# Kernel optimization log

Hardware: AMD Instinct MI355X
Metric: run time of the kernel (lower is better)

The kernel has to match this reference:

```python
import jax, jax.numpy as jnp
import numpy as np

N = 10000        # num_nodes
F_IN = 256       # dataset_num_features
H = 128          # hidden_channels
C_OUT = 40       # dataset_num_classes
L = 3            # num_layers
HEADS = 8
DH = H // HEADS  # per-head dim
E = 160000       # num edges (before self loops)
SCALE = 1.0 / float(np.sqrt(DH))


def setup_inputs() -> dict:
    key = jax.random.key(0)
    ks = jax.random.split(key, 8)
    s = lambda k, *sh: (jax.random.normal(k, sh, dtype=jnp.float32) * 0.05)
    return dict(
        edge_index=jax.random.randint(ks[0], (2, E), 0, N, dtype=jnp.int32),
        x_param=s(ks[1], N, F_IN),
        lin1_w=s(ks[2], F_IN, H),
        lin1_b=jnp.zeros((H,), jnp.float32),
        wq=s(ks[3], L, H, H),
        wk=s(ks[4], L, H, H),
        wv=s(ks[5], L, H, H),
        bq=jnp.zeros((L, H), jnp.float32),
        bk=jnp.zeros((L, H), jnp.float32),
        bv=jnp.zeros((L, H), jnp.float32),
        lin2_w=s(ks[6], H, C_OUT),
        lin2_b=jnp.zeros((C_OUT,), jnp.float32),
    )


def _gcn_norm(edge_index):
    # PyG gcn_norm: add self loops (weight 1), symmetric D^-1/2 A D^-1/2
    loops = jnp.arange(N, dtype=edge_index.dtype)
    row = jnp.concatenate([edge_index[0], loops])  # source j
    col = jnp.concatenate([edge_index[1], loops])  # target i
    deg = jax.ops.segment_sum(jnp.ones(row.shape, jnp.float32), col, num_segments=N)
    dis = jnp.where(deg > 0, jax.lax.rsqrt(jnp.maximum(deg, 1e-12)), 0.0)
    return row, col, dis[row] * dis[col]


def _restricted_softmax(score):
    # softmax with an implicit extra logit at `margin=0`
    m = jnp.maximum(jnp.max(score, axis=-1, keepdims=True), 0.0)
    e = jnp.exp(score - m)
    return e / (jnp.sum(e, axis=-1, keepdims=True) + jnp.exp(-m))


def _forward(edge_index, x_param, lin1_w, lin1_b, wq, wk, wv, bq, bk, bv, lin2_w, lin2_b):
    row, col, norm = _gcn_norm(edge_index)
    # dropouts are eval-mode no-ops
    x = jax.nn.relu(x_param @ lin1_w + lin1_b)  # [N, H]
    x_all = x[:, None, :]                       # [N, 1, H]
    for l in range(L):
        t = x_all.shape[1]
        # project per-node first (linear commutes with per-edge gather)
        q = (x_all[:, -1] @ wq[l] + bq[l]).reshape(N, HEADS, DH)      # query from latest state
        k = (x_all @ wk[l] + bk[l]).reshape(N, t, HEADS, DH)          # keys over full history
        v = (x_all @ wv[l] + bv[l]).reshape(N, t, HEADS, DH)
        qe = q[col]   # [Etot, heads, dh]   (x_i)
        ke = k[row]   # [Etot, t, heads, dh] (x_j)
        ve = v[row]
        score = jnp.einsum('ehd,ethd->eht', qe, ke) * SCALE
        attn = _restricted_softmax(score)        # attention-dropout is a no-op in eval
        msg = jnp.einsum('eht,ethd->ehd', attn, ve).reshape(-1, H) * norm[:, None]
        out = jax.ops.segment_sum(msg, col, num_segments=N)  # aggr='add'
        x = jax.nn.relu(out)
        x_all = jnp.concatenate([x_all, x[:, None, :]], axis=1)
    logits = x_all[:, -1] @ lin2_w + lin2_b
    return jax.nn.log_softmax(logits, axis=1)


def reference(edge_index, x_param, lin1_w, lin1_b, wq, wk, wv, bq, bk, bv, lin2_w, lin2_b):
    return _forward(edge_index, x_param, lin1_w, lin1_b, wq, wk, wv, bq, bk, bv, lin2_w, lin2_b)
```

## Files before the change

### kernel.cpp

```cpp
#include <hip/hip_runtime.h>
#include <math.h>

#define N_NODES 10000
#define F_IN_D  256
#define H_DIM   128
#define C_OUTD  40
#define NHEADS  8
#define NEDGES  160000
#define ETOT    (NEDGES + N_NODES)
#define SCALE_F 0.25f
#define TILES_N 157
#define KVSZ    ((size_t)N_NODES * 3 * 256)

typedef __attribute__((ext_vector_type(8))) short bf16x8;
typedef __attribute__((ext_vector_type(4))) float f32x4;
typedef __attribute__((ext_vector_type(2))) float f32x2;

__device__ __forceinline__ unsigned short f2bf(float f) {
    unsigned int u = __float_as_uint(f);
    unsigned int r = (u + 0x7FFFu + ((u >> 16) & 1u)) >> 16;
    return (unsigned short)r;
}
__device__ __forceinline__ unsigned char f2fp8(float v) {
    int pk = __builtin_amdgcn_cvt_pk_fp8_f32(v, v, 0, false);
    return (unsigned char)(pk & 0xff);
}


__global__ void k_prep(const float* __restrict__ w1, const float* __restrict__ wq,
                       const float* __restrict__ wk, const float* __restrict__ wv,
                       const float* __restrict__ w2, const int* __restrict__ col,
                       unsigned short* __restrict__ W1T, unsigned short* __restrict__ WTq,
                       unsigned short* __restrict__ WTk, unsigned short* __restrict__ WTv,
                       unsigned short* __restrict__ W2T, int* __restrict__ degi,
                       int* __restrict__ cursor) {
    int b = blockIdx.x;
    if (b < 768) {
        int e = b * 256 + threadIdx.x;
        if (e < 32768) {
            int n = e >> 8, k = e & 255;
            W1T[e] = f2bf(w1[k * H_DIM + n]);
        } else if (e < 180224) {
            int e2 = e - 32768;
            int mat = e2 >> 14;
            int r   = e2 & 16383;
            int n = r >> 7, k = r & 127;
            int l = mat / 3, ws = mat % 3;
            const float*    src = (ws == 0) ? wq  : (ws == 1) ? wk  : wv;
            unsigned short* dst = (ws == 0) ? WTq : (ws == 1) ? WTk : WTv;
            dst[l * 16384 + n * H_DIM + k] = f2bf(src[l * 16384 + k * H_DIM + n]);
        } else if (e < 186368) {
            int e3 = e - 180224;
            int c = e3 >> 7, k = e3 & 127;
            W2T[c * H_DIM + k] = (c < C_OUTD) ? f2bf(w2[k * C_OUTD + c]) : 0;
        } else if (e < 196368) {
            cursor[e - 186368] = 0;
        }
    } else {
        int e = (b - 768) * 256 + threadIdx.x;
        if (e < NEDGES) atomicAdd(&degi[col[e]], 1);
    }
}


__device__ __forceinline__ void lin1_block(int bid, int ct0, const float* __restrict__ X,
                                           const unsigned short* __restrict__ W1T,
                                           const float* __restrict__ b1,
                                           unsigned short* __restrict__ X0, int nct) {
    int tid = threadIdx.x;
    int wid = tid >> 6, lane = tid & 63;
    int m = lane & 15, quad = lane >> 4;
    int rowA = bid * 64 + wid * 16 + m;
    int rowc = rowA < N_NODES ? rowA : N_NODES - 1;
    bf16x8 af[8];
    const float* ap = X + (size_t)rowc * F_IN_D + quad * 8;
    #pragma unroll
    for (int s = 0; s < 8; ++s) {
        float4 lo = *(const float4*)(ap + s * 32);
        float4 hi = *(const float4*)(ap + s * 32 + 4);
        union { unsigned short u[8]; bf16x8 v; } pk;
        pk.u[0] = f2bf(lo.x); pk.u[1] = f2bf(lo.y);
        pk.u[2] = f2bf(lo.z); pk.u[3] = f2bf(lo.w);
        pk.u[4] = f2bf(hi.x); pk.u[5] = f2bf(hi.y);
        pk.u[6] = f2bf(hi.z); pk.u[7] = f2bf(hi.w);
        af[s] = pk.v;
    }
    int row0 = bid * 64 + wid * 16 + quad * 4;
    for (int ct = ct0; ct < ct0 + nct; ++ct) {
        int col = ct * 16 + m;
        const unsigned short* bp = W1T + (size_t)col * F_IN_D + quad * 8;
        f32x4 acc = {0.f, 0.f, 0.f, 0.f};
        #pragma unroll
        for (int s = 0; s < 8; ++s) {
            bf16x8 bfr = __builtin_bit_cast(bf16x8, *(const uint4*)(bp + s * 32));
            acc = __builtin_amdgcn_mfma_f32_16x16x32_bf16(af[s], bfr, acc, 0, 0, 0);
        }
        float bb = b1[col];
        #pragma unroll
        for (int rg = 0; rg < 4; ++rg) {
            int r = row0 + rg;
            if (r < N_NODES)
                X0[(size_t)r * H_DIM + col] = f2bf(fmaxf(acc[rg] + bb, 0.f));
        }
    }
}

__device__ __forceinline__ void qkv_block(int mi, int rt,
                                          const unsigned short* __restrict__ XHb,
                                          const unsigned short* __restrict__ WTq_l,
                                          const unsigned short* __restrict__ WTk_l,
                                          const unsigned short* __restrict__ WTv_l,
                                          const float* __restrict__ bq_l,
                                          const float* __restrict__ bk_l,
                                          const float* __restrict__ bv_l,
                                          unsigned short* __restrict__ Qb,
                                          unsigned char* __restrict__ KVb,
                                          int hasQ, int qslice, int nK, int sbase, int nct) {
    int tid = threadIdx.x;
    int wid = tid >> 6, lane = tid & 63;
    int m = lane & 15, quad = lane >> 4;
    const unsigned short* WT; const float* bias; int slice, mode;
    if (hasQ && mi == 0) { WT = WTq_l; bias = bq_l; slice = qslice; mode = 0; }
    else {
        int j = mi - hasQ;
        if (j < nK) { WT = WTk_l; bias = bk_l; slice = sbase + j;      mode = 1; }
        else        { WT = WTv_l; bias = bv_l; slice = sbase + j - nK; mode = 2; }
    }
    const unsigned short* A = XHb + (size_t)slice * N_NODES * H_DIM;
    int rowA = rt * 64 + wid * 16 + m;
    bf16x8 af[4];
    const unsigned short* ap = A + (size_t)rowA * H_DIM + quad * 8;
    #pragma unroll
    for (int s = 0; s < 4; ++s)
        af[s] = __builtin_bit_cast(bf16x8, *(const uint4*)(ap + s * 32));
    int row0 = rt * 64 + wid * 16 + quad * 4;
    int vofs = (mode == 2) ? 8 : 0;
    for (int cp = 0; cp < nct; ++cp) {
        int colA = cp * 32 + m;
        int colB = colA + 16;
        const unsigned short* bpA = WT + (size_t)colA * H_DIM + quad * 8;
        const unsigned short* bpB = WT + (size_t)colB * H_DIM + quad * 8;
        bf16x8 bA[4], bB[4];
        #pragma unroll
        for (int s = 0; s < 4; ++s) {
            bA[s] = __builtin_bit_cast(bf16x8, *(const uint4*)(bpA + s * 32));
            bB[s] = __builtin_bit_cast(bf16x8, *(const uint4*)(bpB + s * 32));
        }
        f32x4 accA = {0.f, 0.f, 0.f, 0.f};
        f32x4 accB = {0.f, 0.f, 0.f, 0.f};
        #pragma unroll
        for (int s = 0; s < 4; ++s) {
            accA = __builtin_amdgcn_mfma_f32_16x16x32_bf16(af[s], bA[s], accA, 0, 0, 0);
            accB = __builtin_amdgcn_mfma_f32_16x16x32_bf16(af[s], bB[s], accB, 0, 0, 0);
        }
        float bbA = bias[colA], bbB = bias[colB];
        #pragma unroll
        for (int rg = 0; rg < 4; ++rg) {
            int r = row0 + rg;
            if (r < N_NODES) {
                float vA = accA[rg] + bbA;
                float vB = accB[rg] + bbB;
                if (mode == 0) {
                    Qb[(size_t)r * H_DIM + colA] = f2bf(vA * SCALE_F);
                    Qb[(size_t)r * H_DIM + colB] = f2bf(vB * SCALE_F);
                } else {
                    size_t nb = ((size_t)r * 3 + slice) * 256;
                    KVb[nb + (colA >> 3) * 16 + (colA & 7) + vofs] = f2fp8(vA);
                    KVb[nb + (colB >> 3) * 16 + (colB & 7) + vofs] = f2fp8(vB);
                }
            }
        }
    }
}


template <int T>
__device__ __forceinline__ void kv_load(const uint4* __restrict__ KV, int r, int ci,
                                        uint4 (&kv)[T]) {
    const uint4* p = KV + (size_t)r * 48 + ci;
    #pragma unroll
    for (int s = 0; s < T; ++s) kv[s] = p[s * 16];
}

template <int T>
__device__ __forceinline__ void edge_accum(const uint4 (&kv)[T], const float (&q)[8],
                                           float nrm, float (&a)[8]) {
    float den = 1.f;
    float mv[8];
    #pragma unroll
    for (int i = 0; i < 8; ++i) mv[i] = 0.f;
    #pragma unroll
    for (int s = 0; s < T; ++s) {
        f32x2 k0 = __builtin_amdgcn_cvt_pk_f32_fp8(kv[s].x, false);
        f32x2 k1 = __builtin_amdgcn_cvt_pk_f32_fp8(kv[s].x, true);
        f32x2 k2 = __builtin_amdgcn_cvt_pk_f32_fp8(kv[s].y, false);
        f32x2 k3 = __builtin_amdgcn_cvt_pk_f32_fp8(kv[s].y, true);
        float p = q[0] * k0[0] + q[1] * k0[1] + q[2] * k1[0] + q[3] * k1[1]
                + q[4] * k2[0] + q[5] * k2[1] + q[6] * k3[0] + q[7] * k3[1];
        p += __shfl_xor(p, 1, 2);
        float w = __expf(p);
        den += w;
        f32x2 v0 = __builtin_amdgcn_cvt_pk_f32_fp8(kv[s].z, false);
        f32x2 v1 = __builtin_amdgcn_cvt_pk_f32_fp8(kv[s].z, true);
        f32x2 v2 = __builtin_amdgcn_cvt_pk_f32_fp8(kv[s].w, false);
        f32x2 v3 = __builtin_amdgcn_cvt_pk_f32_fp8(kv[s].w, true);
        mv[0] += w * v0[0]; mv[1] += w * v0[1];
        mv[2] += w * v1[0]; mv[3] += w * v1[1];
        mv[4] += w * v2[0]; mv[5] += w * v2[1];
        mv[6] += w * v3[0]; mv[7] += w * v3[1];
    }
    float ws = __fdividef(nrm, den);
    #pragma unroll
    for (int i = 0; i < 8; ++i) a[i] += ws * mv[i];
}

template <int T>
__device__ __forceinline__ void attn_block(int bid, const unsigned short* __restrict__ Q,
                                           const uint4* __restrict__ KV,
                                           const int2* __restrict__ csr,
                                           const int* __restrict__ degi,
                                           unsigned int* __restrict__ Xout) {
    int tid = threadIdx.x;
    int wid = tid >> 6, lane = tid & 63;
    int quarter = lane >> 4, ci = lane & 15;
    int n = bid * 4 + wid;

    int cnt = degi[n] + 1;
    if (cnt > 64) cnt = 64;
    int li = lane < cnt ? lane : cnt - 1;
    int2 eAll = csr[(n << 6) + li];
    int   rAll = eAll.x;
    float nAll = (lane < cnt) ? __int_as_float(eAll.y) : 0.f;

    float q[8];
    {
        uint4 qp = *(const uint4*)&Q[(size_t)n * H_DIM + ci * 8];
        q[0] = __uint_as_float(qp.x << 16);
        q[1] = __uint_as_float(qp.x & 0xffff0000u);
        q[2] = __uint_as_float(qp.y << 16);
        q[3] = __uint_as_float(qp.y & 0xffff0000u);
        q[4] = __uint_as_float(qp.z << 16);
        q[5] = __uint_as_float(qp.z & 0xffff0000u);
        q[6] = __uint_as_float(qp.w << 16);
        q[7] = __uint_as_float(qp.w & 0xffff0000u);
    }
    int nq = (cnt + 3) >> 2;
    float a[8];
    #pragma unroll
    for (int i = 0; i < 8; ++i) a[i] = 0.f;

    auto rowN = [&](int j4) { return __shfl(rAll, j4 < 63 ? j4 : 63, 64); };
    auto nrmN = [&](int j4) { return __shfl(nAll, j4 < 63 ? j4 : 63, 64); };

    uint4 kv0[T], kv1[T], kv2[T], kv3[T];
    kv_load<T>(KV, rowN(quarter), ci, kv0);
    kv_load<T>(KV, rowN(4 + quarter), ci, kv1);
    kv_load<T>(KV, rowN(8 + quarter), ci, kv2);
    kv_load<T>(KV, rowN(12 + quarter), ci, kv3);

    int j = 0;
    for (;;) {
        edge_accum<T>(kv0, q, nrmN(j * 4 + quarter), a);
        if (++j >= nq) break;
        kv_load<T>(KV, rowN((j + 3) * 4 + quarter), ci, kv0);
        edge_accum<T>(kv1, q, nrmN(j * 4 + quarter), a);
        if (++j >= nq) break;
        kv_load<T>(KV, rowN((j + 3) * 4 + quarter), ci, kv1);
        edge_accum<T>(kv2, q, nrmN(j * 4 + quarter), a);
        if (++j >= nq) break;
        kv_load<T>(KV, rowN((j + 3) * 4 + quarter), ci, kv2);
        edge_accum<T>(kv3, q, nrmN(j * 4 + quarter), a);
        if (++j >= nq) break;
        kv_load<T>(KV, rowN((j + 3) * 4 + quarter), ci, kv3);
    }

    #pragma unroll
    for (int i = 0; i < 8; ++i) {
        a[i] += __shfl_xor(a[i], 16, 64);
        a[i] += __shfl_xor(a[i], 32, 64);
    }
    if (quarter == 0) {
        uint4 o;
        o.x = ((unsigned int)f2bf(fmaxf(a[1], 0.f)) << 16) | (unsigned int)f2bf(fmaxf(a[0], 0.f));
        o.y = ((unsigned int)f2bf(fmaxf(a[3], 0.f)) << 16) | (unsigned int)f2bf(fmaxf(a[2], 0.f));
        o.z = ((unsigned int)f2bf(fmaxf(a[5], 0.f)) << 16) | (unsigned int)f2bf(fmaxf(a[4], 0.f));
        o.w = ((unsigned int)f2bf(fmaxf(a[7], 0.f)) << 16) | (unsigned int)f2bf(fmaxf(a[6], 0.f));
        *(uint4*)&Xout[(size_t)n * 64 + ci * 4] = o;
    }
}


__global__ __launch_bounds__(256) void k_lin1_scatter(const float* __restrict__ X,
                                                      const unsigned short* __restrict__ W1T,
                                                      const float* __restrict__ b1,
                                                      unsigned short* __restrict__ X0,
                                                      const int* __restrict__ row,
                                                      const int* __restrict__ col,
                                                      const int* __restrict__ degi,
                                                      int* __restrict__ cursor,
                                                      int2* __restrict__ csr, int nct) {
    int b = blockIdx.x;
    if (b < 2 * TILES_N) {
        int rt = b % TILES_N, half = b / TILES_N;
        lin1_block(rt, half * 4, X, W1T, b1, X0, nct);
        return;
    }
    int e = (b - 2 * TILES_N) * 256 + threadIdx.x;
    if (e >= ETOT) return;
    int r, c;
    if (e < NEDGES) { r = row[e]; c = col[e]; }
    else            { r = c = e - NEDGES; }
    int slot = atomicAdd(&cursor[c], 1);
    if (slot > 63) slot = 63;
    float dr = rsqrtf((float)(degi[r] + 1));
    float dc = rsqrtf((float)(degi[c] + 1));
    int2 ent; ent.x = r; ent.y = __float_as_int(dr * dc);
    csr[(c << 6) + slot] = ent;
}

template <int T>
__global__ __launch_bounds__(256) void k_attn_qkvold(const unsigned short* __restrict__ Q,
                                                     const uint4* __restrict__ KV,
                                                     const int2* __restrict__ csr,
                                                     const int* __restrict__ degi,
                                                     unsigned int* __restrict__ Xout,
                                                     const unsigned short* __restrict__ XHb,
                                                     const unsigned short* __restrict__ WTk_l,
                                                     const unsigned short* __restrict__ WTv_l,
                                                     const float* __restrict__ bk_l,
                                                     const float* __restrict__ bv_l,
                                                     unsigned char* __restrict__ KVnext,
                                                     int nK, int nct) {
    if (blockIdx.x < 2500) {
        attn_block<T>(blockIdx.x, Q, KV, csr, degi, Xout);
        return;
    }
    int b = blockIdx.x - 2500;
    qkv_block(b / TILES_N, b % TILES_N, XHb, nullptr, WTk_l, WTv_l,
              nullptr, bk_l, bv_l, nullptr, KVnext, 0, 0, nK, 0, nct);
}

__global__ __launch_bounds__(256) void k_qkv(const unsigned short* __restrict__ XHb,
                                             const unsigned short* __restrict__ WTq_l,
                                             const unsigned short* __restrict__ WTk_l,
                                             const unsigned short* __restrict__ WTv_l,
                                             const float* __restrict__ bq_l,
                                             const float* __restrict__ bk_l,
                                             const float* __restrict__ bv_l,
                                             unsigned short* __restrict__ Qb,
                                             unsigned char* __restrict__ KVb,
                                             int qslice, int nct) {
    qkv_block(blockIdx.x / TILES_N, blockIdx.x % TILES_N, XHb, WTq_l, WTk_l, WTv_l,
              bq_l, bk_l, bv_l, Qb, KVb, 1, qslice, 1, qslice, nct);
}

template <int T>
__global__ __launch_bounds__(256) void k_attn_agg(const unsigned short* __restrict__ Q,
                                                  const uint4* __restrict__ KV,
                                                  const int2* __restrict__ csr,
                                                  const int* __restrict__ degi,
                                                  unsigned int* __restrict__ Xout) {
    attn_block<T>(blockIdx.x, Q, KV, csr, degi, Xout);
}


__global__ __launch_bounds__(128) void k_lin2_mfma(const unsigned short* __restrict__ X,
                                                   const unsigned short* __restrict__ W2T,
                                                   const float* __restrict__ b2,
                                                   float* __restrict__ out) {
    int tid = threadIdx.x;
    int wid = tid >> 6, lane = tid & 63;
    int m = lane & 15, quad = lane >> 4;
    int rowA = blockIdx.x * 32 + wid * 16 + m;
    bf16x8 af[4];
    const unsigned short* ap = X + (size_t)rowA * H_DIM + quad * 8;
    #pragma unroll
    for (int s = 0; s < 4; ++s)
        af[s] = __builtin_bit_cast(bf16x8, *(const uint4*)(ap + s * 32));

    f32x4 acc0 = {0.f, 0.f, 0.f, 0.f};
    f32x4 acc1 = {0.f, 0.f, 0.f, 0.f};
    f32x4 acc2 = {0.f, 0.f, 0.f, 0.f};
    const unsigned short* bp0 = W2T + (size_t)(m)      * H_DIM + quad * 8;
    const unsigned short* bp1 = W2T + (size_t)(16 + m) * H_DIM + quad * 8;
    const unsigned short* bp2 = W2T + (size_t)(32 + m) * H_DIM + quad * 8;
    #pragma unroll
    for (int s = 0; s < 4; ++s) {
        bf16x8 b0 = __builtin_bit_cast(bf16x8, *(const uint4*)(bp0 + s * 32));
        acc0 = __builtin_amdgcn_mfma_f32_16x16x32_bf16(af[s], b0, acc0, 0, 0, 0);
        bf16x8 b1 = __builtin_bit_cast(bf16x8, *(const uint4*)(bp1 + s * 32));
        acc1 = __builtin_amdgcn_mfma_f32_16x16x32_bf16(af[s], b1, acc1, 0, 0, 0);
        bf16x8 b2f = __builtin_bit_cast(bf16x8, *(const uint4*)(bp2 + s * 32));
        acc2 = __builtin_amdgcn_mfma_f32_16x16x32_bf16(af[s], b2f, acc2, 0, 0, 0);
    }

    float bb0 = b2[m], bb1 = b2[16 + m];
    float bb2 = (m < 8) ? b2[32 + m] : 0.f;
    int row0 = blockIdx.x * 32 + wid * 16 + quad * 4;
    #pragma unroll
    for (int rg = 0; rg < 4; ++rg) {
        int r = row0 + rg;
        float v0 = acc0[rg] + bb0;
        float v1 = acc1[rg] + bb1;
        float v2 = (m < 8) ? (acc2[rg] + bb2) : -INFINITY;
        float mx = fmaxf(fmaxf(v0, v1), v2);
        #pragma unroll
        for (int o = 8; o > 0; o >>= 1) mx = fmaxf(mx, __shfl_xor(mx, o, 16));
        float sm = __expf(v0 - mx) + __expf(v1 - mx) + ((m < 8) ? __expf(v2 - mx) : 0.f);
        #pragma unroll
        for (int o = 8; o > 0; o >>= 1) sm += __shfl_xor(sm, o, 16);
        float lse = mx + __logf(sm);
        if (r < N_NODES) {
            out[(size_t)r * C_OUTD + m]      = v0 - lse;
            out[(size_t)r * C_OUTD + 16 + m] = v1 - lse;
            if (m < 8) out[(size_t)r * C_OUTD + 32 + m] = v2 - lse;
        }
    }
}


extern "C" void kernel_launch(void* const* d_in, const int* in_sizes, int n_in,
                              void* d_out, int out_size, void* d_ws, size_t ws_size,
                              hipStream_t stream) {
    const int*   ei      = (const int*)d_in[0];
    const int*   row     = ei;
    const int*   col     = ei + NEDGES;
    const float* x_param = (const float*)d_in[1];
    const float* lin1_w  = (const float*)d_in[2];
    const float* lin1_b  = (const float*)d_in[3];
    const float* wq      = (const float*)d_in[4];
    const float* wk      = (const float*)d_in[5];
    const float* wv      = (const float*)d_in[6];
    const float* bq      = (const float*)d_in[7];
    const float* bk      = (const float*)d_in[8];
    const float* bv      = (const float*)d_in[9];
    const float* lin2_w  = (const float*)d_in[10];
    const float* lin2_b  = (const float*)d_in[11];
    float*       out     = (float*)d_out;

    char* wbase = (char*)d_ws;
    size_t off = 0;
    auto alloc = [&](size_t bytes) -> void* {
        off = (off + 255) & ~(size_t)255;
        void* p = wbase + off;
        off += bytes;
        return p;
    };
    int*            degi     = (int*)           alloc((size_t)N_NODES * 4);
    int*            cursor   = (int*)           alloc((size_t)N_NODES * 4);
    int2*           csr      = (int2*)          alloc((size_t)N_NODES * 64 * 8);
    unsigned short* W1T      = (unsigned short*)alloc((size_t)H_DIM * F_IN_D * 2);
    unsigned short* WTq      = (unsigned short*)alloc((size_t)3 * H_DIM * H_DIM * 2);
    unsigned short* WTk      = (unsigned short*)alloc((size_t)3 * H_DIM * H_DIM * 2);
    unsigned short* WTv      = (unsigned short*)alloc((size_t)3 * H_DIM * H_DIM * 2);
    unsigned short* W2T      = (unsigned short*)alloc((size_t)48 * H_DIM * 2);
    unsigned short* XHb      = (unsigned short*)alloc((size_t)4 * N_NODES * H_DIM * 2);
    unsigned short* Qb       = (unsigned short*)alloc((size_t)N_NODES * H_DIM * 2);
    unsigned char*  KVb      = (unsigned char*) alloc(2 * KVSZ);

    hipMemsetAsync(degi, 0, (size_t)N_NODES * 4, stream);
    k_prep<<<1393, 256, 0, stream>>>(lin1_w, wq, wk, wv, lin2_w, col,
                                     W1T, WTq, WTk, WTv, W2T, degi, cursor);

    k_lin1_scatter<<<2 * TILES_N + 665, 256, 0, stream>>>(
        x_param, W1T, lin1_b, XHb, row, col, degi, cursor, csr, 4);

    k_qkv<<<3 * TILES_N, 256, 0, stream>>>(
        XHb, WTq, WTk, WTv, bq, bk, bv, Qb, KVb, 0, 4);

    unsigned int* X1 = (unsigned int*)(XHb + (size_t)1 * N_NODES * H_DIM);
    unsigned int* X2 = (unsigned int*)(XHb + (size_t)2 * N_NODES * H_DIM);
    unsigned int* X3 = (unsigned int*)(XHb + (size_t)3 * N_NODES * H_DIM);

    k_attn_qkvold<1><<<2500 + 2 * TILES_N, 256, 0, stream>>>(
        Qb, (const uint4*)KVb, csr, degi, X1,
        XHb, WTk + 16384, WTv + 16384, bk + H_DIM, bv + H_DIM,
        KVb + KVSZ, 1, 4);

    k_qkv<<<3 * TILES_N, 256, 0, stream>>>(
        XHb, WTq + 16384, WTk + 16384, WTv + 16384,
        bq + H_DIM, bk + H_DIM, bv + H_DIM, Qb, KVb + KVSZ, 1, 4);

    k_attn_qkvold<2><<<2500 + 4 * TILES_N, 256, 0, stream>>>(
        Qb, (const uint4*)(KVb + KVSZ), csr, degi, X2,
        XHb, WTk + 2 * 16384, WTv + 2 * 16384, bk + 2 * H_DIM, bv + 2 * H_DIM,
        KVb, 2, 4);

    k_qkv<<<3 * TILES_N, 256, 0, stream>>>(
        XHb, WTq + 2 * 16384, WTk + 2 * 16384, WTv + 2 * 16384,
        bq + 2 * H_DIM, bk + 2 * H_DIM, bv + 2 * H_DIM, Qb, KVb, 2, 4);

    k_attn_agg<3><<<2500, 256, 0, stream>>>(Qb, (const uint4*)KVb, csr, degi, X3);

    k_lin2_mfma<<<313, 128, 0, stream>>>(XHb + (size_t)3 * N_NODES * H_DIM,
                                         W2T, lin2_b, out);
}
```

Measured before the change: 226.7 us.

## Restructure graph-prep pipeline: reuse degree-atomic slots, fuse scatter with layer-0 QKV

```diff
diff --git a/kernel.cpp b/kernel.cpp
--- a/kernel.cpp
+++ b/kernel.cpp
@@ -27,38 +27,54 @@
 }
 
 
-__global__ void k_prep(const float* __restrict__ w1, const float* __restrict__ wq,
-                       const float* __restrict__ wk, const float* __restrict__ wv,
-                       const float* __restrict__ w2, const int* __restrict__ col,
-                       unsigned short* __restrict__ W1T, unsigned short* __restrict__ WTq,
-                       unsigned short* __restrict__ WTk, unsigned short* __restrict__ WTv,
-                       unsigned short* __restrict__ W2T, int* __restrict__ degi,
-                       int* __restrict__ cursor) {
-    int b = blockIdx.x;
-    if (b < 768) {
-        int e = b * 256 + threadIdx.x;
-        if (e < 32768) {
-            int n = e >> 8, k = e & 255;
-            W1T[e] = f2bf(w1[k * H_DIM + n]);
-        } else if (e < 180224) {
-            int e2 = e - 32768;
-            int mat = e2 >> 14;
-            int r   = e2 & 16383;
-            int n = r >> 7, k = r & 127;
-            int l = mat / 3, ws = mat % 3;
-            const float*    src = (ws == 0) ? wq  : (ws == 1) ? wk  : wv;
-            unsigned short* dst = (ws == 0) ? WTq : (ws == 1) ? WTk : WTv;
-            dst[l * 16384 + n * H_DIM + k] = f2bf(src[l * 16384 + k * H_DIM + n]);
-        } else if (e < 186368) {
-            int e3 = e - 180224;
-            int c = e3 >> 7, k = e3 & 127;
-            W2T[c * H_DIM + k] = (c < C_OUTD) ? f2bf(w2[k * C_OUTD + c]) : 0;
-        } else if (e < 196368) {
-            cursor[e - 186368] = 0;
-        }
-    } else {
-        int e = (b - 768) * 256 + threadIdx.x;
-        if (e < NEDGES) atomicAdd(&degi[col[e]], 1);
+__global__ __launch_bounds__(256) void k_prep_cast(const float* __restrict__ w1,
+                                                   const float* __restrict__ wq,
+                                                   const float* __restrict__ wk,
+                                                   const float* __restrict__ wv,
+                                                   const float* __restrict__ w2,
+                                                   unsigned short* __restrict__ W1T,
+                                                   unsigned short* __restrict__ WTq,
+                                                   unsigned short* __restrict__ WTk,
+                                                   unsigned short* __restrict__ WTv,
+                                                   unsigned short* __restrict__ W2T,
+                                                   int* __restrict__ degi) {
+    int t = blockIdx.x * 256 + threadIdx.x;
+    if (t < 8192) {
+        float4 v = *(const float4*)(w1 + 4 * t);
+        int e = 4 * t;
+        #pragma unroll
+        for (int i = 0; i < 4; ++i) {
+            int k = (e + i) >> 7, n = (e + i) & 127;
+            W1T[n * 256 + k] = f2bf(((const float*)&v)[i]);
+        }
+    } else if (t < 45056) {
+        int u = t - 8192;
+        int mat = u >> 12;
+        int l = mat / 3, ws = mat % 3;
+        const float*    src = (ws == 0) ? wq  : (ws == 1) ? wk  : wv;
+        unsigned short* dst = (ws == 0) ? WTq : (ws == 1) ? WTk : WTv;
+        int e2 = (u & 4095) * 4;
+        float4 v = *(const float4*)(src + l * 16384 + e2);
+        #pragma unroll
+        for (int i = 0; i < 4; ++i) {
+            int k = (e2 + i) >> 7, n = (e2 + i) & 127;
+            dst[l * 16384 + n * 128 + k] = f2bf(((const float*)&v)[i]);
+        }
+    } else if (t < 46336) {
+        int e = (t - 45056) * 4;
+        float4 v = *(const float4*)(w2 + e);
+        #pragma unroll
+        for (int i = 0; i < 4; ++i) {
+            int ee = e + i;
+            int k = ee / 40, c = ee - k * 40;
+            W2T[c * 128 + k] = f2bf(((const float*)&v)[i]);
+        }
+    } else if (t < 46592) {
+        int idx = 5120 + (t - 46336) * 4;
+        *(uint2*)&W2T[idx] = make_uint2(0u, 0u);
+    } else if (t < 49092) {
+        int idx = (t - 46592) * 4;
+        *(int4*)&degi[idx] = make_int4(0, 0, 0, 0);
     }
 }
 
@@ -290,32 +306,54 @@
 }
 
 
-__global__ __launch_bounds__(256) void k_lin1_scatter(const float* __restrict__ X,
-                                                      const unsigned short* __restrict__ W1T,
-                                                      const float* __restrict__ b1,
-                                                      unsigned short* __restrict__ X0,
-                                                      const int* __restrict__ row,
+__global__ __launch_bounds__(256) void k_deg_lin1(const int* __restrict__ col,
+                                                  int* __restrict__ degi,
+                                                  int* __restrict__ slotbuf,
+                                                  const float* __restrict__ X,
+                                                  const unsigned short* __restrict__ W1T,
+                                                  const float* __restrict__ b1,
+                                                  unsigned short* __restrict__ X0, int nct) {
+    int b = blockIdx.x;
+    if (b < 625) {
+        int e = b * 256 + threadIdx.x;
+        slotbuf[e] = atomicAdd(&degi[col[e]], 1);
+        return;
+    }
+    int bid = b - 625;
+    lin1_block(bid % TILES_N, (bid / TILES_N) * 4, X, W1T, b1, X0, nct);
+}
+
+__global__ __launch_bounds__(256) void k_scatter_qkv0(const int* __restrict__ row,
                                                       const int* __restrict__ col,
                                                       const int* __restrict__ degi,
-                                                      int* __restrict__ cursor,
-                                                      int2* __restrict__ csr, int nct) {
-    int b = blockIdx.x;
-    if (b < 2 * TILES_N) {
-        int rt = b % TILES_N, half = b / TILES_N;
-        lin1_block(rt, half * 4, X, W1T, b1, X0, nct);
+                                                      const int* __restrict__ slotbuf,
+                                                      int2* __restrict__ csr,
+                                                      const unsigned short* __restrict__ XHb,
+                                                      const unsigned short* __restrict__ WTq,
+                                                      const unsigned short* __restrict__ WTk,
+                                                      const unsigned short* __restrict__ WTv,
+                                                      const float* __restrict__ bq,
+                                                      const float* __restrict__ bk,
+                                                      const float* __restrict__ bv,
+                                                      unsigned short* __restrict__ Qb,
+                                                      unsigned char* __restrict__ KVb,
+                                                      int nct) {
+    if (blockIdx.x < 665) {
+        int e = blockIdx.x * 256 + threadIdx.x;
+        if (e >= ETOT) return;
+        int r, c, slot;
+        if (e < NEDGES) { r = row[e]; c = col[e]; slot = slotbuf[e]; }
+        else            { r = c = e - NEDGES; slot = degi[c]; }
+        if (slot > 63) slot = 63;
+        float dr = rsqrtf((float)(degi[r] + 1));
+        float dc = rsqrtf((float)(degi[c] + 1));
+        int2 ent; ent.x = r; ent.y = __float_as_int(dr * dc);
+        csr[(c << 6) + slot] = ent;
         return;
     }
-    int e = (b - 2 * TILES_N) * 256 + threadIdx.x;
-    if (e >= ETOT) return;
-    int r, c;
-    if (e < NEDGES) { r = row[e]; c = col[e]; }
-    else            { r = c = e - NEDGES; }
-    int slot = atomicAdd(&cursor[c], 1);
-    if (slot > 63) slot = 63;
-    float dr = rsqrtf((float)(degi[r] + 1));
-    float dc = rsqrtf((float)(degi[c] + 1));
-    int2 ent; ent.x = r; ent.y = __float_as_int(dr * dc);
-    csr[(c << 6) + slot] = ent;
+    int b = blockIdx.x - 665;
+    qkv_block(b / TILES_N, b % TILES_N, XHb, WTq, WTk, WTv, bq, bk, bv,
+              Qb, KVb, 1, 0, 1, 0, nct);
 }
 
 template <int T>
@@ -447,7 +485,7 @@
         return p;
     };
     int*            degi     = (int*)           alloc((size_t)N_NODES * 4);
-    int*            cursor   = (int*)           alloc((size_t)N_NODES * 4);
+    int*            slotbuf  = (int*)           alloc((size_t)NEDGES * 4);
     int2*           csr      = (int2*)          alloc((size_t)N_NODES * 64 * 8);
     unsigned short* W1T      = (unsigned short*)alloc((size_t)H_DIM * F_IN_D * 2);
     unsigned short* WTq      = (unsigned short*)alloc((size_t)3 * H_DIM * H_DIM * 2);
@@ -458,15 +496,15 @@
     unsigned short* Qb       = (unsigned short*)alloc((size_t)N_NODES * H_DIM * 2);
     unsigned char*  KVb      = (unsigned char*) alloc(2 * KVSZ);
 
-    hipMemsetAsync(degi, 0, (size_t)N_NODES * 4, stream);
-    k_prep<<<1393, 256, 0, stream>>>(lin1_w, wq, wk, wv, lin2_w, col,
-                                     W1T, WTq, WTk, WTv, W2T, degi, cursor);
-
-    k_lin1_scatter<<<2 * TILES_N + 665, 256, 0, stream>>>(
-        x_param, W1T, lin1_b, XHb, row, col, degi, cursor, csr, 4);
-
-    k_qkv<<<3 * TILES_N, 256, 0, stream>>>(
-        XHb, WTq, WTk, WTv, bq, bk, bv, Qb, KVb, 0, 4);
+    k_prep_cast<<<192, 256, 0, stream>>>(lin1_w, wq, wk, wv, lin2_w,
+                                         W1T, WTq, WTk, WTv, W2T, degi);
+
+    k_deg_lin1<<<939, 256, 0, stream>>>(col, degi, slotbuf,
+                                        x_param, W1T, lin1_b, XHb, 4);
+
+    k_scatter_qkv0<<<665 + 3 * TILES_N, 256, 0, stream>>>(
+        row, col, degi, slotbuf, csr,
+        XHb, WTq, WTk, WTv, bq, bk, bv, Qb, KVb, 4);
 
     unsigned int* X1 = (unsigned int*)(XHb + (size_t)1 * N_NODES * H_DIM);
     unsigned int* X2 = (unsigned int*)(XHb + (size_t)2 * N_NODES * H_DIM);
```

Result: faster. 219.4 us (-3.2%).
